# Optimization experiments

Measured on AMD Instinct MI355X. Metric: run time of the kernel, lower is better.

The kernel has to match this reference:

```python
import jax, jax.numpy as jnp
import numpy as np

IMG = 800          # image size (square)
STRIDE = 4         # feature-map stride
S = 14             # rcnn_crop_size
C = 256            # crop_channels
N = 512            # number of rpn proposals
NUM_CLASSES = 81   # COCO (incl. background at index 0)
HID = 1024
NMS_TH = 0.5
SCORE_TH = 0.05


def setup_inputs() -> dict:
    key = jax.random.key(0)
    ks = jax.random.split(key, 8)
    features = jax.random.normal(ks[0], (1, C, IMG // STRIDE, IMG // STRIDE), jnp.float32)
    # valid proposal boxes (x0, y0, x1, y1) in image coordinates
    u = jax.random.uniform(ks[1], (N, 4), jnp.float32)
    x0 = u[:, 0] * (IMG - 64.0)
    y0 = u[:, 1] * (IMG - 64.0)
    bw = 16.0 + u[:, 2] * 240.0
    bh = 16.0 + u[:, 3] * 240.0
    proposals = jnp.stack([x0, y0, jnp.minimum(x0 + bw, IMG - 1.0), jnp.minimum(y0 + bh, IMG - 1.0)], axis=1)
    d1 = C * S * S  # 50176
    w1 = jax.random.normal(ks[2], (d1, HID), jnp.float32) * (1.0 / np.sqrt(d1))
    b1 = jnp.zeros((HID,), jnp.float32)
    w2 = jax.random.normal(ks[3], (HID, HID), jnp.float32) * (1.0 / np.sqrt(HID))
    b2 = jnp.zeros((HID,), jnp.float32)
    w_cls = jax.random.normal(ks[4], (HID, NUM_CLASSES), jnp.float32) * (1.0 / np.sqrt(HID))
    b_cls = jnp.zeros((NUM_CLASSES,), jnp.float32)
    w_reg = jax.random.normal(ks[5], (HID, NUM_CLASSES * 4), jnp.float32) * (1.0 / np.sqrt(HID))
    b_reg = jnp.zeros((NUM_CLASSES * 4,), jnp.float32)
    return dict(features=features, proposals=proposals, w1=w1, b1=b1, w2=w2, b2=b2,
                w_cls=w_cls, b_cls=b_cls, w_reg=w_reg, b_reg=b_reg)


def roi_align(feat, boxes):
    """feat: [C,H,W]; boxes: [N,4] image coords -> crops [N,C,S,S] via bilinear sampling (1 sample per bin)."""
    _, H, W = feat.shape
    b = boxes / STRIDE
    t = (jnp.arange(S, dtype=feat.dtype) + 0.5) / S                # [S] bin centers
    xs = b[:, 0:1] + (b[:, 2:3] - b[:, 0:1]) * t                   # [N,S]
    ys = b[:, 1:2] + (b[:, 3:4] - b[:, 1:2]) * t                   # [N,S]
    xx = jnp.broadcast_to(xs[:, None, :], (boxes.shape[0], S, S))  # [N,S,S]
    yy = jnp.broadcast_to(ys[:, :, None], (boxes.shape[0], S, S))
    x0f = jnp.floor(xx); y0f = jnp.floor(yy)
    fx = xx - x0f; fy = yy - y0f
    x0i = jnp.clip(x0f.astype(jnp.int32), 0, W - 1); x1i = jnp.clip(x0i + 1, 0, W - 1)
    y0i = jnp.clip(y0f.astype(jnp.int32), 0, H - 1); y1i = jnp.clip(y0i + 1, 0, H - 1)
    # gathers -> [C,N,S,S]
    v = (((1 - fx) * (1 - fy))[None] * feat[:, y0i, x0i]
         + (fx * (1 - fy))[None] * feat[:, y0i, x1i]
         + ((1 - fx) * fy)[None] * feat[:, y1i, x0i]
         + (fx * fy)[None] * feat[:, y1i, x1i])
    return v.transpose(1, 0, 2, 3)  # [N,C,S,S]


def decode_boxes(rois, d):
    w = rois[:, 2] - rois[:, 0]; h = rois[:, 3] - rois[:, 1]
    cx = rois[:, 0] + 0.5 * w; cy = rois[:, 1] + 0.5 * h
    px = cx + d[:, 0] * w; py = cy + d[:, 1] * h
    pw = w * jnp.exp(jnp.clip(d[:, 2], -4.0, 4.0))
    ph = h * jnp.exp(jnp.clip(d[:, 3], -4.0, 4.0))
    b = jnp.stack([px - 0.5 * pw, py - 0.5 * ph, px + 0.5 * pw, py + 0.5 * ph], axis=1)
    return jnp.clip(b, 0.0, IMG - 1.0)


def iou_matrix(b):
    area = jnp.maximum(b[:, 2] - b[:, 0], 0.0) * jnp.maximum(b[:, 3] - b[:, 1], 0.0)
    ix0 = jnp.maximum(b[:, None, 0], b[None, :, 0])
    iy0 = jnp.maximum(b[:, None, 1], b[None, :, 1])
    ix1 = jnp.minimum(b[:, None, 2], b[None, :, 2])
    iy1 = jnp.minimum(b[:, None, 3], b[None, :, 3])
    inter = jnp.maximum(ix1 - ix0, 0.0) * jnp.maximum(iy1 - iy0, 0.0)
    return inter / (area[:, None] + area[None, :] - inter + 1e-6)


def reference(features, proposals, w1, b1, w2, b2, w_cls, b_cls, w_reg, b_reg):
    # 1) RoIAlign crop
    crops = roi_align(features[0], proposals)              # [N,C,S,S]
    # 2) RCNN head
    x = crops.reshape(N, -1)
    x = jax.nn.relu(x @ w1 + b1)
    x = jax.nn.relu(x @ w2 + b2)
    logits = x @ w_cls + b_cls                             # [N,81]
    deltas = (x @ w_reg + b_reg).reshape(N, NUM_CLASSES, 4)
    # 3) NMS post-processing
    probs = jax.nn.softmax(logits, axis=-1)
    fg = probs[:, 1:]                                      # exclude background
    labels = jnp.argmax(fg, axis=-1) + 1                   # [N]
    scores = jnp.max(fg, axis=-1)                          # [N]
    d = deltas[jnp.arange(N), labels]                      # per-ROI delta of predicted class
    boxes = decode_boxes(proposals, d)
    order = jnp.argsort(-scores)
    bs = boxes[order]; ss = scores[order]; ls = labels[order]
    valid = ss > SCORE_TH
    M = iou_matrix(bs)                                     # [N,N]
    idx = jnp.arange(N)
    def body(i, keep):
        alive = keep[i] & valid[i]
        supp = (M[i] > NMS_TH) & (idx > i) & alive
        return keep & (~supp)
    keep = jax.lax.fori_loop(0, N, body, valid)
    keepf = jax.lax.stop_gradient(keep.astype(bs.dtype))
    final = jnp.concatenate([bs, ss[:, None]], axis=1) * keepf[:, None]   # [N,5]
    return final, ls.astype(jnp.int32), keep
```

## Files before the change

kernel.cpp:

```cpp
#include <hip/hip_runtime.h>
#include <cstdint>

#define F_H 200
#define F_W 200
#define D1  50176
#define NBOX 512
#define NHID 1024

typedef _Float16 f16;
typedef _Float16 half8 __attribute__((ext_vector_type(8)));
typedef _Float16 half4v __attribute__((ext_vector_type(4)));
typedef _Float16 half2v __attribute__((ext_vector_type(2)));
typedef float    f32x4 __attribute__((ext_vector_type(4)));

__device__ __forceinline__ void gload16(const void* g, void* l) {
  __builtin_amdgcn_global_load_lds((const __attribute__((address_space(1))) void*)g,
                                   (__attribute__((address_space(3))) void*)l,
                                   16, 0, 0);
}

__device__ __forceinline__ half2v pkrtz(float a, float b) {
  return __builtin_bit_cast(half2v, __builtin_amdgcn_cvt_pkrtz(a, b));
}

__device__ __forceinline__ void splitf16(float v, f16& h, f16& l) {
  f16 hh = (f16)v;
  float hf = (float)hh;
  if (fabsf(hf) < 6.1035156e-5f) hf = 0.f;
  h = (f16)hf;
  l = (f16)((v - hf) * 2048.f);
}

__global__ __launch_bounds__(256) void k_roi(const float* __restrict__ feat,
                                             const float* __restrict__ prop,
                                             f16* __restrict__ xhi, f16* __restrict__ xlo) {
  uint32_t idx = blockIdx.x * 256u + threadIdx.x;
  uint32_t n = idx / 25088u;
  uint32_t rem = idx % 25088u;
  uint32_t c = rem / 98u;
  uint32_t r2 = rem % 98u;
  uint32_t i = r2 / 7u;
  uint32_t jp = r2 % 7u;
  float b0 = prop[n * 4 + 0] * 0.25f, b1 = prop[n * 4 + 1] * 0.25f;
  float b2 = prop[n * 4 + 2] * 0.25f, b3 = prop[n * 4 + 3] * 0.25f;
  float ty = ((float)i + 0.5f) * (1.0f / 14.0f);
  float yy = b1 + (b3 - b1) * ty;
  float y0f = floorf(yy);
  float fy = yy - y0f;
  int y0 = (int)y0f; y0 = y0 < 0 ? 0 : (y0 > F_H - 1 ? F_H - 1 : y0);
  int y1 = y0 + 1 > F_H - 1 ? F_H - 1 : y0 + 1;
  const float* fr0 = feat + (size_t)c * (F_H * F_W) + (size_t)y0 * F_W;
  const float* fr1 = feat + (size_t)c * (F_H * F_W) + (size_t)y1 * F_W;
  f16 hs[2], ls[2];
#pragma unroll
  for (int e = 0; e < 2; ++e) {
    uint32_t j = jp * 2u + (uint32_t)e;
    float tx = ((float)j + 0.5f) * (1.0f / 14.0f);
    float xx = b0 + (b2 - b0) * tx;
    float x0f = floorf(xx);
    float fx = xx - x0f;
    int x0 = (int)x0f; x0 = x0 < 0 ? 0 : (x0 > F_W - 1 ? F_W - 1 : x0);
    int x1 = x0 + 1 > F_W - 1 ? F_W - 1 : x0 + 1;
    float v00 = fr0[x0], v01 = fr0[x1], v10 = fr1[x0], v11 = fr1[x1];
    float v = (1.f - fx) * (1.f - fy) * v00 + fx * (1.f - fy) * v01 +
              (1.f - fx) * fy * v10 + fx * fy * v11;
    splitf16(v, hs[e], ls[e]);
  }
  uint32_t base = n * 50176u + c * 196u + i * 14u + jp * 2u;
  half2v hv; hv[0] = hs[0]; hv[1] = hs[1];
  half2v lv; lv[0] = ls[0]; lv[1] = ls[1];
  *(half2v*)(xhi + base) = hv;
  *(half2v*)(xlo + base) = lv;
}

__global__ __launch_bounds__(256) void k_pack(const float* __restrict__ wc, const float* __restrict__ bc,
                                              const float* __restrict__ wr, const float* __restrict__ br,
                                              float* __restrict__ wh, float* __restrict__ bh) {
  uint32_t idx = blockIdx.x * 256u + threadIdx.x;
  if (idx < (uint32_t)NHID * 512u) {
    uint32_t k = idx >> 9, n = idx & 511u;
    float v = 0.f;
    if (n < 81u) v = wc[k * 81u + n];
    else if (n < 405u) v = wr[k * 324u + (n - 81u)];
    wh[idx] = v;
  } else if (idx < (uint32_t)NHID * 512u + 512u) {
    uint32_t n = idx - (uint32_t)NHID * 512u;
    float v = 0.f;
    if (n < 81u) v = bc[n];
    else if (n < 405u) v = br[n - 81u];
    bh[n] = v;
  }
}

__global__ __launch_bounds__(512, 2) void k_gemm(
    const f16* __restrict__ Ahi, const f16* __restrict__ Alo,
    const float* __restrict__ B, float* __restrict__ Cp,
    int K, int N, int Kc, int nMt, int nNt)
{
  __shared__ char sm[131072];
  const int t = threadIdx.x;
  const int lane = t & 63;
  const int wid = t >> 6;
  const int wr = wid >> 2;
  const int wc = wid & 3;
  const int rl = lane & 15;
  const int lq = lane >> 4;

  int bid = blockIdx.x;
  int low = bid & 7, q = bid >> 3;
  int nt = q % nNt;
  int chi = q / nNt;
  int c = chi * 8 + low;
  int ks = c / nMt;
  int mt = c % nMt;
  const int brow = mt * 256;
  const int nbase = nt * 256;
  const int k0 = ks * Kc;
  const int nk = Kc >> 5;

  uint32_t aoffg[2], aldso[2];
#pragma unroll
  for (int i = 0; i < 2; ++i) {
    uint32_t idx = (uint32_t)t + 512u * i;
    uint32_t r = idx >> 2, s = idx & 3;
    uint32_t sz = s ^ ((r >> 1) & 3);
    aoffg[i] = (uint32_t)(brow + r) * (uint32_t)K + sz * 8u;
    aldso[i] = idx * 16u;
  }
  uint32_t boffg[2][2], bldso[2][2];
#pragma unroll
  for (int h = 0; h < 2; ++h)
#pragma unroll
    for (int i = 0; i < 2; ++i) {
      uint32_t idx = (uint32_t)t + 512u * i;
      uint32_t kr = idx >> 5, sg = idx & 31;
      uint32_t sgs = sg ^ (((kr >> 3) & 3) << 2);
      boffg[h][i] = kr * (uint32_t)N + (uint32_t)(nbase + h * 128) + sgs * 4u;
      bldso[h][i] = 32768u + (uint32_t)h * 16384u + idx * 16u;
    }

  const uint32_t a_off = (uint32_t)(wr * 8192 + rl * 64) + (uint32_t)((lq ^ ((rl >> 1) & 3)) * 16);
  const uint32_t b_lane = (uint32_t)((((wc ^ lq) & 3) * 16 + rl) * 4);

  f32x4 zero4 = {0.f, 0.f, 0.f, 0.f};
  f32x4 acc[8][4];
#pragma unroll
  for (int m = 0; m < 8; ++m)
#pragma unroll
    for (int n = 0; n < 4; ++n) acc[m][n] = zero4;

#define STAGE_A(LB, KB) do { \
    gload16(Ahi + aoffg[0] + (KB), (LB) + aldso[0]); \
    gload16(Alo + aoffg[0] + (KB), (LB) + 16384 + aldso[0]); \
    gload16(Ahi + aoffg[1] + (KB), (LB) + aldso[1]); \
    gload16(Alo + aoffg[1] + (KB), (LB) + 16384 + aldso[1]); \
  } while (0)

#define STAGE_B(LB, KB) do { \
    gload16(B + (size_t)(KB) * (uint32_t)N + boffg[0][0], (LB) + bldso[0][0]); \
    gload16(B + (size_t)(KB) * (uint32_t)N + boffg[0][1], (LB) + bldso[0][1]); \
    gload16(B + (size_t)(KB) * (uint32_t)N + boffg[1][0], (LB) + bldso[1][0]); \
    gload16(B + (size_t)(KB) * (uint32_t)N + boffg[1][1], (LB) + bldso[1][1]); \
  } while (0)

#define COMPUTE_PHASE(P) do { \
    half8 bhv[2], blv[2]; \
    _Pragma("unroll") \
    for (int x = 0; x < 2; ++x) { \
      const int nf = 2 * (P) + x; \
      const char* bb = lb + 32768 + (nf >> 1) * 16384 + (nf & 1) * 256 + b_lane; \
      _Pragma("unroll") \
      for (int jj = 0; jj < 8; jj += 2) { \
        float v0 = *(const float*)(bb + (lq * 8 + jj) * 512); \
        float v1 = *(const float*)(bb + (lq * 8 + jj + 1) * 512); \
        half2v hp = pkrtz(v0, v1); \
        f16 e0 = (fabsf(v0) >= 6.1035156e-5f) ? hp[0] : (f16)0; \
        f16 e1 = (fabsf(v1) >= 6.1035156e-5f) ? hp[1] : (f16)0; \
        half2v lp = pkrtz((v0 - (float)e0) * 2048.f, (v1 - (float)e1) * 2048.f); \
        bhv[x][jj] = e0; bhv[x][jj + 1] = e1; \
        blv[x][jj] = lp[0]; blv[x][jj + 1] = lp[1]; \
      } \
    } \
    __builtin_amdgcn_s_setprio(1); \
    _Pragma("unroll") \
    for (int m = 0; m < 8; ++m) { \
      half8 ah = *(const half8*)(lb + a_off + m * 1024); \
      half8 al = *(const half8*)(lb + 16384 + a_off + m * 1024); \
      _Pragma("unroll") \
      for (int x = 0; x < 2; ++x) { \
        const int nf = 2 * (P) + x; \
        acc[m][nf] = __builtin_amdgcn_mfma_f32_16x16x32_f16(ah, bhv[x], acc[m][nf], 0, 0, 0); \
        f32x4 tt = __builtin_amdgcn_mfma_f32_16x16x32_f16(ah, blv[x], zero4, 0, 0, 0); \
        tt = __builtin_amdgcn_mfma_f32_16x16x32_f16(al, bhv[x], tt, 0, 0, 0); \
        acc[m][nf] += tt * 4.8828125e-4f; \
      } \
    } \
    __builtin_amdgcn_s_setprio(0); \
  } while (0)

  STAGE_A(sm, (uint32_t)k0);
  STAGE_B(sm, (uint32_t)k0);

  int cur = 0;
  for (int kt = 0; kt < nk; ++kt) {
    int ktn = (kt + 1 < nk) ? kt + 1 : kt;
    uint32_t kbn = (uint32_t)(k0 + ktn * 32);
    const char* lb = sm + cur * 65536;
    char* lbn = sm + (cur ^ 1) * 65536;

    asm volatile("s_waitcnt vmcnt(2)" ::: "memory");
    __builtin_amdgcn_s_barrier();
    __builtin_amdgcn_sched_barrier(0);
    STAGE_A(lbn, kbn);
    COMPUTE_PHASE(0);

    asm volatile("s_waitcnt vmcnt(4)" ::: "memory");
    __builtin_amdgcn_s_barrier();
    __builtin_amdgcn_sched_barrier(0);
    STAGE_B(lbn, kbn);
    COMPUTE_PHASE(1);

    cur ^= 1;
  }

  float* Cs = Cp + (size_t)ks * ((size_t)512 * (uint32_t)N);
#pragma unroll
  for (int m = 0; m < 8; ++m) {
    int rg = brow + wr * 128 + m * 16 + lq * 4;
#pragma unroll
    for (int nf = 0; nf < 4; ++nf) {
      int cg = nbase + nf * 64 + wc * 16 + rl;
#pragma unroll
      for (int rr = 0; rr < 4; ++rr)
        Cs[(size_t)(rg + rr) * (uint32_t)N + cg] = acc[m][nf][rr];
    }
  }
#undef STAGE_A
#undef STAGE_B
#undef COMPUTE_PHASE
}

__global__ __launch_bounds__(256) void k_reduce(
    const float* __restrict__ parts, const float* __restrict__ bias,
    int nS, int MN4, int Ncols, int relu,
    float* __restrict__ outf, f16* __restrict__ ohi, f16* __restrict__ olo)
{
  uint32_t idx = blockIdx.x * 256u + threadIdx.x;
  if (idx >= (uint32_t)MN4) return;
  f32x4 s = *(const f32x4*)(bias + ((idx * 4u) % (uint32_t)Ncols));
  const f32x4* p4 = (const f32x4*)parts;
  for (int i = 0; i < nS; ++i) s += p4[(size_t)i * (uint32_t)MN4 + idx];
  if (relu) {
#pragma unroll
    for (int j = 0; j < 4; ++j) s[j] = fmaxf(s[j], 0.f);
  }
  if (outf) *(f32x4*)(outf + (size_t)idx * 4) = s;
  if (ohi) {
    half4v h, l;
#pragma unroll
    for (int j = 0; j < 4; ++j) { f16 hh, ll; splitf16(s[j], hh, ll); h[j] = hh; l[j] = ll; }
    *(half4v*)(ohi + (size_t)idx * 4) = h;
    *(half4v*)(olo + (size_t)idx * 4) = l;
  }
}

__global__ __launch_bounds__(256) void k_post(
    const float* __restrict__ ld, const float* __restrict__ prop,
    float* __restrict__ boxes, float* __restrict__ scores, int* __restrict__ labels)
{
  int n = blockIdx.x * 256 + threadIdx.x;
  if (n >= NBOX) return;
  const float* L = ld + (size_t)n * 512;
  float m = L[0];
  for (int j = 1; j < 81; ++j) m = fmaxf(m, L[j]);
  float sum = 0.f;
  for (int j = 0; j < 81; ++j) sum += expf(L[j] - m);
  float best = -1.f; int bj = 1;
  for (int j = 1; j < 81; ++j) {
    float p = expf(L[j] - m) / sum;
    if (p > best) { best = p; bj = j; }
  }
  float d0 = L[81 + bj * 4 + 0];
  float d1 = L[81 + bj * 4 + 1];
  float d2 = L[81 + bj * 4 + 2];
  float d3 = L[81 + bj * 4 + 3];
  float p0 = prop[n * 4 + 0], p1 = prop[n * 4 + 1], p2 = prop[n * 4 + 2], p3 = prop[n * 4 + 3];
  float w = p2 - p0, h = p3 - p1;
  float cx = p0 + 0.5f * w, cy = p1 + 0.5f * h;
  float px = cx + d0 * w, py = cy + d1 * h;
  float pw = w * expf(fminf(fmaxf(d2, -4.f), 4.f));
  float ph = h * expf(fminf(fmaxf(d3, -4.f), 4.f));
  float bx0 = px - 0.5f * pw, by0 = py - 0.5f * ph;
  float bx1 = px + 0.5f * pw, by1 = py + 0.5f * ph;
  boxes[n * 4 + 0] = fminf(fmaxf(bx0, 0.f), 799.f);
  boxes[n * 4 + 1] = fminf(fmaxf(by0, 0.f), 799.f);
  boxes[n * 4 + 2] = fminf(fmaxf(bx1, 0.f), 799.f);
  boxes[n * 4 + 3] = fminf(fmaxf(by1, 0.f), 799.f);
  scores[n] = best;
  labels[n] = bj;
}

__global__ __launch_bounds__(512) void k_sort(
    const float* __restrict__ scores, const float* __restrict__ boxes, const int* __restrict__ labels,
    float* __restrict__ bs, float* __restrict__ ss, int* __restrict__ ls)
{
  __shared__ unsigned long long keys[512];
  int t = threadIdx.x;
  unsigned sb = __float_as_uint(scores[t]);
  keys[t] = ((unsigned long long)(0xFFFFFFFFu - sb) << 32) | (unsigned)t;
  __syncthreads();
  for (int k = 2; k <= 512; k <<= 1) {
    for (int j = k >> 1; j > 0; j >>= 1) {
      int p = t ^ j;
      if (p > t) {
        unsigned long long a = keys[t], b = keys[p];
        bool asc = ((t & k) == 0);
        if (asc ? (a > b) : (a < b)) { keys[t] = b; keys[p] = a; }
      }
      __syncthreads();
    }
  }
  unsigned o = (unsigned)(keys[t] & 0xFFFFFFFFu);
  ss[t] = scores[o];
  ls[t] = labels[o];
  bs[t * 4 + 0] = boxes[o * 4 + 0];
  bs[t * 4 + 1] = boxes[o * 4 + 1];
  bs[t * 4 + 2] = boxes[o * 4 + 2];
  bs[t * 4 + 3] = boxes[o * 4 + 3];
}

__global__ __launch_bounds__(64) void k_mask(const float* __restrict__ bs,
                                             unsigned long long* __restrict__ mask) {
  int i = blockIdx.x;
  int lane = threadIdx.x;
  float ax0 = bs[i * 4], ay0 = bs[i * 4 + 1], ax1 = bs[i * 4 + 2], ay1 = bs[i * 4 + 3];
  float aarea = fmaxf(ax1 - ax0, 0.f) * fmaxf(ay1 - ay0, 0.f);
  for (int w = 0; w < 8; ++w) {
    int j = w * 64 + lane;
    float bx0 = bs[j * 4], by0 = bs[j * 4 + 1], bx1 = bs[j * 4 + 2], by1 = bs[j * 4 + 3];
    float barea = fmaxf(bx1 - bx0, 0.f) * fmaxf(by1 - by0, 0.f);
    float ix0 = fmaxf(ax0, bx0), iy0 = fmaxf(ay0, by0);
    float ix1 = fminf(ax1, bx1), iy1 = fminf(ay1, by1);
    float inter = fmaxf(ix1 - ix0, 0.f) * fmaxf(iy1 - iy0, 0.f);
    float iou = inter / (aarea + barea - inter + 1e-6f);
    bool cond = (iou > 0.5f) && (j > i);
    unsigned long long b = __ballot(cond);
    if (lane == 0) mask[i * 8 + w] = b;
  }
}

__global__ __launch_bounds__(64) void k_nms(const unsigned long long* __restrict__ mask,
                                            const float* __restrict__ ss,
                                            const float* __restrict__ bs,
                                            const int* __restrict__ ls,
                                            float* __restrict__ out) {
  int lane = threadIdx.x;
  unsigned long long bal[8];
  for (int w = 0; w < 8; ++w) bal[w] = __ballot(ss[w * 64 + lane] > 0.05f);
  unsigned long long keep = (lane < 8) ? bal[lane] : 0ULL;
  for (int i = 0; i < 512; ++i) {
    unsigned long long kw = __shfl(keep, i >> 6);
    if ((kw >> (i & 63)) & 1ULL) {
      unsigned long long mi = (lane < 8) ? mask[i * 8 + lane] : 0ULL;
      keep &= ~mi;
    }
  }
  __shared__ unsigned long long kws[8];
  if (lane < 8) kws[lane] = keep;
  __syncthreads();
  for (int it = 0; it < 56; ++it) {
    int idx = lane + it * 64;
    float val;
    if (idx < 2560) {
      int i = idx / 5, c2 = idx % 5;
      bool kb = (kws[i >> 6] >> (i & 63)) & 1ULL;
      val = kb ? (c2 < 4 ? bs[i * 4 + c2] : ss[i]) : 0.f;
    } else if (idx < 3072) {
      int i = idx - 2560;
      val = (float)ls[i];
    } else {
      int i = idx - 3072;
      val = ((kws[i >> 6] >> (i & 63)) & 1ULL) ? 1.f : 0.f;
    }
    out[idx] = val;
  }
}

static constexpr size_t SZ_X    = (size_t)NBOX * D1 * 2;
static constexpr size_t OFF_XHI = 0;
static constexpr size_t OFF_XLO = OFF_XHI + SZ_X;
static constexpr size_t OFF_PART = OFF_XLO + SZ_X;
static constexpr size_t SZ_PART = (size_t)32 * 512 * 1024 * 4;
static constexpr size_t SZ_H    = (size_t)512 * 1024 * 2;
static constexpr size_t OFF_H1HI = OFF_PART + SZ_PART;
static constexpr size_t OFF_H1LO = OFF_H1HI + SZ_H;
static constexpr size_t OFF_H2HI = OFF_H1LO + SZ_H;
static constexpr size_t OFF_H2LO = OFF_H2HI + SZ_H;
static constexpr size_t OFF_WH   = OFF_H2LO + SZ_H;
static constexpr size_t OFF_BH   = OFF_WH + (size_t)1024 * 512 * 4;
static constexpr size_t OFF_LD   = OFF_BH + 4096;
static constexpr size_t OFF_BOX  = OFF_LD + (size_t)512 * 512 * 4;
static constexpr size_t OFF_SC   = OFF_BOX + 512 * 4 * 4;
static constexpr size_t OFF_LB   = OFF_SC + 4096;
static constexpr size_t OFF_BS   = OFF_LB + 4096;
static constexpr size_t OFF_SS   = OFF_BS + 512 * 4 * 4;
static constexpr size_t OFF_LS   = OFF_SS + 4096;
static constexpr size_t OFF_MASK = OFF_LS + 4096;
static constexpr size_t OFF_END  = OFF_MASK + (size_t)512 * 8 * 8;

extern "C" void kernel_launch(void* const* d_in, const int* in_sizes, int n_in,
                              void* d_out, int out_size, void* d_ws, size_t ws_size,
                              hipStream_t stream)
{
  (void)in_sizes; (void)n_in;
  const float* feat = (const float*)d_in[0];
  const float* prop = (const float*)d_in[1];
  const float* w1   = (const float*)d_in[2];
  const float* b1   = (const float*)d_in[3];
  const float* w2   = (const float*)d_in[4];
  const float* b2   = (const float*)d_in[5];
  const float* wcls = (const float*)d_in[6];
  const float* bcls = (const float*)d_in[7];
  const float* wreg = (const float*)d_in[8];
  const float* breg = (const float*)d_in[9];
  float* out = (float*)d_out;
  char* W = (char*)d_ws;

  if (ws_size < OFF_END) {
    (void)hipMemsetAsync(out, 0x7f, (size_t)out_size * 4, stream);
    return;
  }

  f16*   xhi   = (f16*)(W + OFF_XHI);
  f16*   xlo   = (f16*)(W + OFF_XLO);
  float* parts = (float*)(W + OFF_PART);
  f16*   h1hi  = (f16*)(W + OFF_H1HI);
  f16*   h1lo  = (f16*)(W + OFF_H1LO);
  f16*   h2hi  = (f16*)(W + OFF_H2HI);
  f16*   h2lo  = (f16*)(W + OFF_H2LO);
  float* whead = (float*)(W + OFF_WH);
  float* bhead = (float*)(W + OFF_BH);
  float* ldbuf = (float*)(W + OFF_LD);
  float* boxes = (float*)(W + OFF_BOX);
  float* scores= (float*)(W + OFF_SC);
  int*   labels= (int*)(W + OFF_LB);
  float* bsrt  = (float*)(W + OFF_BS);
  float* ssrt  = (float*)(W + OFF_SS);
  int*   lsrt  = (int*)(W + OFF_LS);
  unsigned long long* maskb = (unsigned long long*)(W + OFF_MASK);

  k_pack<<<2050, 256, 0, stream>>>(wcls, bcls, wreg, breg, whead, bhead);
  k_roi<<<50176, 256, 0, stream>>>(feat, prop, xhi, xlo);

  k_gemm<<<256, 512, 0, stream>>>(xhi, xlo, w1, parts, D1, 1024, 1568, 2, 4);
  k_reduce<<<512, 256, 0, stream>>>(parts, b1, 32, 131072, 1024, 1, nullptr, h1hi, h1lo);

  k_gemm<<<64, 512, 0, stream>>>(h1hi, h1lo, w2, parts, 1024, 1024, 128, 2, 4);
  k_reduce<<<512, 256, 0, stream>>>(parts, b2, 8, 131072, 1024, 1, nullptr, h2hi, h2lo);

  k_gemm<<<64, 512, 0, stream>>>(h2hi, h2lo, whead, parts, 1024, 512, 64, 2, 2);
  k_reduce<<<256, 256, 0, stream>>>(parts, bhead, 16, 65536, 512, 0, ldbuf, nullptr, nullptr);

  k_post<<<2, 256, 0, stream>>>(ldbuf, prop, boxes, scores, labels);
  k_sort<<<1, 512, 0, stream>>>(scores, boxes, labels, bsrt, ssrt, lsrt);
  k_mask<<<512, 64, 0, stream>>>(bsrt, maskb);
  k_nms<<<1, 64, 0, stream>>>(maskb, ssrt, bsrt, lsrt, out);
}
```

Before: 415.8 us.

## Pre-split and transpose weights to fp16 hi/lo for a new GEMM

Adds a transpose-and-split kernel that turns the fp32 weight matrices into transposed fp16 hi/lo pairs in workspace. A new GEMM kernel then loads both A and B straight into LDS with async global-to-LDS copies, instead of converting fp32 B inside the GEMM. This path runs whenever the workspace is large enough. It adds an extra pass over the 200MB w1 on every call (read fp32, write two fp16 copies), so the benefit depends on whether the cheaper GEMM inner loop outweighs that traffic.

```diff
diff --git a/kernel.cpp b/kernel.cpp
--- a/kernel.cpp
+++ b/kernel.cpp
@@ -27,7 +27,8 @@
   f16 hh = (f16)v;
   float hf = (float)hh;
   if (fabsf(hf) < 6.1035156e-5f) hf = 0.f;
-  h = (f16)hf;
+  h = (f16)hh;
+  if (fabsf(hf) < 6.1035156e-5f) h = (f16)0.f;
   l = (f16)((v - hf) * 2048.f);
 }
 
@@ -73,6 +74,58 @@
   *(half2v*)(xlo + base) = lv;
 }
 
+__global__ __launch_bounds__(256) void k_tsplit(const float* __restrict__ W,
+                                                f16* __restrict__ hiT, f16* __restrict__ loT,
+                                                int Kdim, int Ndim) {
+  __shared__ f16 lh[64 * 72];
+  __shared__ f16 ll[64 * 72];
+  int t = threadIdx.x;
+  int k0 = blockIdx.x * 64, n0 = blockIdx.y * 64;
+  int r = t >> 2, cq = t & 3;
+  const float* src = W + (size_t)(k0 + r) * Ndim + n0 + cq * 16;
+  f16 hv[16], lv[16];
+#pragma unroll
+  for (int e = 0; e < 4; ++e) {
+    f32x4 v = *(const f32x4*)(src + e * 4);
+#pragma unroll
+    for (int x = 0; x < 4; ++x) splitf16(v[x], hv[e * 4 + x], lv[e * 4 + x]);
+  }
+#pragma unroll
+  for (int j = 0; j < 16; ++j) {
+    int n_l = cq * 16 + j;
+    lh[n_l * 72 + r] = hv[j];
+    ll[n_l * 72 + r] = lv[j];
+  }
+  __syncthreads();
+  f16* oh = hiT + (size_t)(n0 + r) * Kdim + k0 + cq * 16;
+  f16* ol = loT + (size_t)(n0 + r) * Kdim + k0 + cq * 16;
+  *(half8*)(oh)     = *(const half8*)(&lh[r * 72 + cq * 16]);
+  *(half8*)(oh + 8) = *(const half8*)(&lh[r * 72 + cq * 16 + 8]);
+  *(half8*)(ol)     = *(const half8*)(&ll[r * 72 + cq * 16]);
+  *(half8*)(ol + 8) = *(const half8*)(&ll[r * 72 + cq * 16 + 8]);
+}
+
+__global__ __launch_bounds__(256) void k_packT(const float* __restrict__ wc_, const float* __restrict__ bc,
+                                               const float* __restrict__ wr_, const float* __restrict__ br,
+                                               f16* __restrict__ whT_hi, f16* __restrict__ whT_lo,
+                                               float* __restrict__ bh) {
+  uint32_t idx = blockIdx.x * 256u + threadIdx.x;
+  if (idx < 512u * 1024u) {
+    uint32_t n = idx >> 10, k = idx & 1023u;
+    float v = 0.f;
+    if (n < 81u) v = wc_[k * 81u + n];
+    else if (n < 405u) v = wr_[k * 324u + (n - 81u)];
+    f16 h, l; splitf16(v, h, l);
+    whT_hi[idx] = h; whT_lo[idx] = l;
+  } else if (idx < 512u * 1024u + 512u) {
+    uint32_t n = idx - 512u * 1024u;
+    float v = 0.f;
+    if (n < 81u) v = bc[n];
+    else if (n < 405u) v = br[n - 81u];
+    bh[n] = v;
+  }
+}
+
 __global__ __launch_bounds__(256) void k_pack(const float* __restrict__ wc, const float* __restrict__ bc,
                                               const float* __restrict__ wr, const float* __restrict__ br,
                                               float* __restrict__ wh, float* __restrict__ bh) {
@@ -90,6 +143,143 @@
     else if (n < 405u) v = br[n - 81u];
     bh[n] = v;
   }
+}
+
+__global__ __launch_bounds__(512, 2) void k_gemm2(
+    const f16* __restrict__ Ahi, const f16* __restrict__ Alo,
+    const f16* __restrict__ Bhi, const f16* __restrict__ Blo,
+    float* __restrict__ Cp, int K, int N, int Kc, int nMt, int nNt)
+{
+  __shared__ char sm[131072];
+  const int t = threadIdx.x;
+  const int lane = t & 63;
+  const int wid = t >> 6;
+  const int wr = wid >> 2;
+  const int wc = wid & 3;
+  const int rl = lane & 15;
+  const int lq = lane >> 4;
+
+  int bid = blockIdx.x;
+  int low = bid & 7, qq = bid >> 3;
+  int nt = qq % nNt;
+  int chi = qq / nNt;
+  int c = chi * 8 + low;
+  int ks = c / nMt;
+  int mt = c % nMt;
+  const int brow = mt * 256;
+  const int nbase = nt * 256;
+  const int k0 = ks * Kc;
+  const int nk = Kc >> 5;
+
+  uint32_t aoffg[2], aldso[2];
+#pragma unroll
+  for (int i = 0; i < 2; ++i) {
+    uint32_t idx = (uint32_t)t + 512u * i;
+    uint32_t q2 = idx >> 2, s = idx & 3;
+    uint32_t qh = q2 >> 6;
+    uint32_t grh = (qh == 1u) ? 2u : (qh == 2u) ? 1u : qh;
+    uint32_t gr = grh * 64u + (q2 & 63u);
+    aoffg[i] = (uint32_t)(brow + gr) * (uint32_t)K + (s ^ ((q2 >> 1) & 3u)) * 8u;
+    aldso[i] = idx * 16u;
+  }
+  uint32_t boffg[2], bldso[2];
+#pragma unroll
+  for (int i = 0; i < 2; ++i) {
+    uint32_t idx = (uint32_t)t + 512u * i;
+    uint32_t rB = idx >> 2, s = idx & 3;
+    boffg[i] = (uint32_t)(nbase + rB) * (uint32_t)K + (s ^ ((rB >> 1) & 3u)) * 8u;
+    bldso[i] = idx * 16u;
+  }
+
+  const uint32_t swzk = (uint32_t)(lq ^ ((rl >> 1) & 3)) * 16u;
+  const uint32_t a_off_lane = (uint32_t)(rl * 64) + swzk;
+  const uint32_t b_off_lane = (uint32_t)((wc * 16 + rl) * 64) + swzk;
+
+  f32x4 zero4 = {0.f, 0.f, 0.f, 0.f};
+  f32x4 acc[8][4];
+#pragma unroll
+  for (int m = 0; m < 8; ++m)
+#pragma unroll
+    for (int n = 0; n < 4; ++n) acc[m][n] = zero4;
+
+#define PH0STAGE(LB, KB) do { \
+    gload16(Bhi + boffg[0] + (KB), (LB) + 32768 + bldso[0]); \
+    gload16(Blo + boffg[0] + (KB), (LB) + 49152 + bldso[0]); \
+    gload16(Bhi + boffg[1] + (KB), (LB) + 32768 + bldso[1]); \
+    gload16(Blo + boffg[1] + (KB), (LB) + 49152 + bldso[1]); \
+    gload16(Ahi + aoffg[0] + (KB), (LB) + aldso[0]); \
+    gload16(Alo + aoffg[0] + (KB), (LB) + 16384 + aldso[0]); \
+  } while (0)
+
+#define PH1STAGE(LB, KB) do { \
+    gload16(Ahi + aoffg[1] + (KB), (LB) + aldso[1]); \
+    gload16(Alo + aoffg[1] + (KB), (LB) + 16384 + aldso[1]); \
+  } while (0)
+
+#define COMPUTE_PHASE(P) do { \
+    half8 bh2[4], bl2[4]; \
+    _Pragma("unroll") \
+    for (int nf = 0; nf < 4; ++nf) { \
+      bh2[nf] = *(const half8*)(lb + 32768 + nf * 4096 + b_off_lane); \
+      bl2[nf] = *(const half8*)(lb + 49152 + nf * 4096 + b_off_lane); \
+    } \
+    __builtin_amdgcn_s_setprio(1); \
+    _Pragma("unroll") \
+    for (int mm = 0; mm < 4; ++mm) { \
+      const char* ab = lb + (P) * 8192 + wr * 4096 + mm * 1024 + a_off_lane; \
+      half8 ah = *(const half8*)(ab); \
+      half8 al = *(const half8*)(ab + 16384); \
+      _Pragma("unroll") \
+      for (int nf = 0; nf < 4; ++nf) { \
+        acc[(P)*4+mm][nf] = __builtin_amdgcn_mfma_f32_16x16x32_f16(ah, bh2[nf], acc[(P)*4+mm][nf], 0, 0, 0); \
+        f32x4 tt = __builtin_amdgcn_mfma_f32_16x16x32_f16(ah, bl2[nf], zero4, 0, 0, 0); \
+        tt = __builtin_amdgcn_mfma_f32_16x16x32_f16(al, bh2[nf], tt, 0, 0, 0); \
+        acc[(P)*4+mm][nf] += tt * 4.8828125e-4f; \
+      } \
+    } \
+    __builtin_amdgcn_s_setprio(0); \
+  } while (0)
+
+  PH0STAGE(sm, (uint32_t)k0);
+  PH1STAGE(sm, (uint32_t)k0);
+
+  int cur = 0;
+  for (int kt = 0; kt < nk; ++kt) {
+    int ktn = (kt + 1 < nk) ? kt + 1 : kt;
+    uint32_t kbn = (uint32_t)(k0 + ktn * 32);
+    const char* lb = sm + cur * 65536;
+    char* lbn = sm + (cur ^ 1) * 65536;
+
+    asm volatile("s_waitcnt vmcnt(2)" ::: "memory");
+    __builtin_amdgcn_s_barrier();
+    __builtin_amdgcn_sched_barrier(0);
+    PH0STAGE(lbn, kbn);
+    COMPUTE_PHASE(0);
+
+    asm volatile("s_waitcnt vmcnt(6)" ::: "memory");
+    __builtin_amdgcn_s_barrier();
+    __builtin_amdgcn_sched_barrier(0);
+    PH1STAGE(lbn, kbn);
+    COMPUTE_PHASE(1);
+
+    cur ^= 1;
+  }
+
+  float* Cs = Cp + (size_t)ks * ((size_t)512 * (uint32_t)N);
+#pragma unroll
+  for (int m = 0; m < 8; ++m) {
+    int rg = brow + wr * 128 + m * 16 + lq * 4;
+#pragma unroll
+    for (int nf = 0; nf < 4; ++nf) {
+      int cg = nbase + nf * 64 + wc * 16 + rl;
+#pragma unroll
+      for (int rr = 0; rr < 4; ++rr)
+        Cs[(size_t)(rg + rr) * (uint32_t)N + cg] = acc[m][nf][rr];
+    }
+  }
+#undef PH0STAGE
+#undef PH1STAGE
+#undef COMPUTE_PHASE
 }
 
 __global__ __launch_bounds__(512, 2) void k_gemm(
@@ -408,6 +598,31 @@
 static constexpr size_t OFF_MASK = OFF_LS + 4096;
 static constexpr size_t OFF_END  = OFF_MASK + (size_t)512 * 8 * 8;
 
+static constexpr size_t SZ_W1P   = (size_t)1024 * D1 * 2;
+static constexpr size_t NP_XHI   = 0;
+static constexpr size_t NP_XLO   = NP_XHI + SZ_X;
+static constexpr size_t NP_W1HIT = NP_XLO + SZ_X;
+static constexpr size_t NP_W1LOT = NP_W1HIT + SZ_W1P;
+static constexpr size_t NP_PART  = NP_W1LOT + SZ_W1P;
+static constexpr size_t NP_W2HIT = NP_PART + SZ_PART;
+static constexpr size_t NP_W2LOT = NP_W2HIT + (size_t)1024 * 1024 * 2;
+static constexpr size_t NP_WHHIT = NP_W2LOT + (size_t)1024 * 1024 * 2;
+static constexpr size_t NP_WHLOT = NP_WHHIT + (size_t)512 * 1024 * 2;
+static constexpr size_t NP_BH    = NP_WHLOT + (size_t)512 * 1024 * 2;
+static constexpr size_t NP_H1HI  = NP_BH + 4096;
+static constexpr size_t NP_H1LO  = NP_H1HI + SZ_H;
+static constexpr size_t NP_H2HI  = NP_H1LO + SZ_H;
+static constexpr size_t NP_H2LO  = NP_H2HI + SZ_H;
+static constexpr size_t NP_LD    = NP_H2LO + SZ_H;
+static constexpr size_t NP_BOX   = NP_LD + (size_t)512 * 512 * 4;
+static constexpr size_t NP_SC    = NP_BOX + 512 * 4 * 4;
+static constexpr size_t NP_LB    = NP_SC + 4096;
+static constexpr size_t NP_BS    = NP_LB + 4096;
+static constexpr size_t NP_SS    = NP_BS + 512 * 4 * 4;
+static constexpr size_t NP_LS    = NP_SS + 4096;
+static constexpr size_t NP_MASK  = NP_LS + 4096;
+static constexpr size_t NP_END   = NP_MASK + (size_t)512 * 8 * 8;
+
 extern "C" void kernel_launch(void* const* d_in, const int* in_sizes, int n_in,
                               void* d_out, int out_size, void* d_ws, size_t ws_size,
                               hipStream_t stream)
@@ -426,6 +641,51 @@
   float* out = (float*)d_out;
   char* W = (char*)d_ws;
 
+  if (ws_size >= NP_END) {
+    f16*   xhi   = (f16*)(W + NP_XHI);
+    f16*   xlo   = (f16*)(W + NP_XLO);
+    f16*   w1hiT = (f16*)(W + NP_W1HIT);
+    f16*   w1loT = (f16*)(W + NP_W1LOT);
+    float* parts = (float*)(W + NP_PART);
+    f16*   w2hiT = (f16*)(W + NP_W2HIT);
+    f16*   w2loT = (f16*)(W + NP_W2LOT);
+    f16*   whHiT = (f16*)(W + NP_WHHIT);
+    f16*   whLoT = (f16*)(W + NP_WHLOT);
+    float* bhead = (float*)(W + NP_BH);
+    f16*   h1hi  = (f16*)(W + NP_H1HI);
+    f16*   h1lo  = (f16*)(W + NP_H1LO);
+    f16*   h2hi  = (f16*)(W + NP_H2HI);
+    f16*   h2lo  = (f16*)(W + NP_H2LO);
+    float* ldbuf = (float*)(W + NP_LD);
+    float* boxes = (float*)(W + NP_BOX);
+    float* scores= (float*)(W + NP_SC);
+    int*   labels= (int*)(W + NP_LB);
+    float* bsrt  = (float*)(W + NP_BS);
+    float* ssrt  = (float*)(W + NP_SS);
+    int*   lsrt  = (int*)(W + NP_LS);
+    unsigned long long* maskb = (unsigned long long*)(W + NP_MASK);
+
+    k_tsplit<<<dim3(D1 / 64, 1024 / 64), 256, 0, stream>>>(w1, w1hiT, w1loT, D1, 1024);
+    k_roi<<<50176, 256, 0, stream>>>(feat, prop, xhi, xlo);
+    k_tsplit<<<dim3(1024 / 64, 1024 / 64), 256, 0, stream>>>(w2, w2hiT, w2loT, 1024, 1024);
+    k_packT<<<2050, 256, 0, stream>>>(wcls, bcls, wreg, breg, whHiT, whLoT, bhead);
+
+    k_gemm2<<<256, 512, 0, stream>>>(xhi, xlo, w1hiT, w1loT, parts, D1, 1024, 1568, 2, 4);
+    k_reduce<<<512, 256, 0, stream>>>(parts, b1, 32, 131072, 1024, 1, nullptr, h1hi, h1lo);
+
+    k_gemm2<<<256, 512, 0, stream>>>(h1hi, h1lo, w2hiT, w2loT, parts, 1024, 1024, 32, 2, 4);
+    k_reduce<<<512, 256, 0, stream>>>(parts, b2, 32, 131072, 1024, 1, nullptr, h2hi, h2lo);
+
+    k_gemm2<<<128, 512, 0, stream>>>(h2hi, h2lo, whHiT, whLoT, parts, 1024, 512, 32, 2, 2);
+    k_reduce<<<256, 256, 0, stream>>>(parts, bhead, 32, 65536, 512, 0, ldbuf, nullptr, nullptr);
+
+    k_post<<<2, 256, 0, stream>>>(ldbuf, prop, boxes, scores, labels);
+    k_sort<<<1, 512, 0, stream>>>(scores, boxes, labels, bsrt, ssrt, lsrt);
+    k_mask<<<512, 64, 0, stream>>>(bsrt, maskb);
+    k_nms<<<1, 64, 0, stream>>>(maskb, ssrt, bsrt, lsrt, out);
+    return;
+  }
+
   if (ws_size < OFF_END) {
     (void)hipMemsetAsync(out, 0x7f, (size_t)out_size * 4, stream);
     return;
```

Result: slower. 477.9 us (+14.9%).
